# Performance work log

Hardware: AMD Instinct MI355X
Metric: run time of the kernel (lower is better)

The kernel has to match this reference:

```python
import jax, jax.numpy as jnp
import numpy as np

D_IN, D_K, D_V = 1024, 128, 128
B, S = 8, 4096


def setup_inputs() -> dict:
    key = jax.random.key(0)
    kq, kk, kv, kwq, kwk, kwv = jax.random.split(key, 6)
    q = jax.random.normal(kq, (B, S, D_IN), dtype=jnp.float32)
    k = jax.random.normal(kk, (B, S, D_IN), dtype=jnp.float32)
    v = jax.random.normal(kv, (B, S, D_IN), dtype=jnp.float32)
    # nn.Linear(d_in, d_out, bias=None): weight shape [d_out, d_in], y = x @ W^T
    scale = 1.0 / np.sqrt(D_IN)
    Wq = jax.random.uniform(kwq, (D_K, D_IN), jnp.float32, -scale, scale)
    Wk = jax.random.uniform(kwk, (D_K, D_IN), jnp.float32, -scale, scale)
    Wv = jax.random.uniform(kwv, (D_V, D_IN), jnp.float32, -scale, scale)
    return {"q": q, "k": k, "v": v, "Wq": Wq, "Wk": Wk, "Wv": Wv}


def reference(q, k, v, Wq, Wk, Wv):
    # Bias-free projections: [b, s, d_in] @ [d_in, d_k/d_v]
    qh = jnp.einsum('bsd,kd->bsk', q, Wq)
    kh = jnp.einsum('bsd,kd->bsk', k, Wk)
    vh = jnp.einsum('bsd,vd->bsv', v, Wv)
    scores = jnp.einsum('bqk,bsk->bqs', qh, kh) / jnp.sqrt(jnp.float32(D_K))
    attn = jax.nn.softmax(scores, axis=-1)  # [b, s_q, s_kv]
    return jnp.einsum('bqs,bsv->bqv', attn, vh)
```

## Files before the change

kernel.cpp:

```cpp
#include <hip/hip_runtime.h>
#include <hip/hip_bf16.h>
#include <stdint.h>

#define D_IN 1024
#define D_K  128
#define NBATCH 8
#define SEQ  4096
#define MROWS (NBATCH * SEQ)

typedef __attribute__((ext_vector_type(8))) short bf16x8;
typedef __attribute__((ext_vector_type(4))) float f32x4;

__device__ __forceinline__ unsigned short f32_to_bf16(float x) {
    union { float f; uint32_t u; } v; v.f = x;
    uint32_t r = 0x7FFFu + ((v.u >> 16) & 1u);
    return (unsigned short)((v.u + r) >> 16);
}

__device__ __forceinline__ bf16x8 cvt8(float4 lo, float4 hi) {
    bf16x8 r;
    r[0] = (short)f32_to_bf16(lo.x); r[1] = (short)f32_to_bf16(lo.y);
    r[2] = (short)f32_to_bf16(lo.z); r[3] = (short)f32_to_bf16(lo.w);
    r[4] = (short)f32_to_bf16(hi.x); r[5] = (short)f32_to_bf16(hi.y);
    r[6] = (short)f32_to_bf16(hi.z); r[7] = (short)f32_to_bf16(hi.w);
    return r;
}

__device__ __forceinline__ void gload16(const void* src, void* lds) {
    __builtin_amdgcn_global_load_lds(
        (const __attribute__((address_space(1))) void*)src,
        (__attribute__((address_space(3))) void*)lds, 16, 0, 0);
}

__global__ __launch_bounds__(256)
void wconv_kernel(const float* __restrict__ Wq, const float* __restrict__ Wk,
                  const float* __restrict__ Wv, unsigned short* __restrict__ Wt)
{
    const int t  = blockIdx.x * 256 + threadIdx.x;
    const int n  = t & 127;
    const int kc = (t >> 7) & 127;
    const int p  = t >> 14;
    const float* __restrict__ W = (p == 0) ? Wq : (p == 1) ? Wk : Wv;
    const float sc = (p == 0) ? (1.44269504088896f * 0.0883883476483184f) : 1.0f;
    const float4* src = reinterpret_cast<const float4*>(W + (size_t)n * D_IN + kc * 8);
    float4 a = src[0], b = src[1];
    uint4 o;
    o.x = (uint32_t)f32_to_bf16(a.x * sc) | ((uint32_t)f32_to_bf16(a.y * sc) << 16);
    o.y = (uint32_t)f32_to_bf16(a.z * sc) | ((uint32_t)f32_to_bf16(a.w * sc) << 16);
    o.z = (uint32_t)f32_to_bf16(b.x * sc) | ((uint32_t)f32_to_bf16(b.y * sc) << 16);
    o.w = (uint32_t)f32_to_bf16(b.z * sc) | ((uint32_t)f32_to_bf16(b.w * sc) << 16);
    *reinterpret_cast<uint4*>(Wt + (size_t)t * 8) = o;
}

#define RBM 32

__global__ __launch_bounds__(256, 3)
void proj_kernel(const float* __restrict__ Xq, const float* __restrict__ Xk,
                 const float* __restrict__ Xv,
                 const unsigned short* __restrict__ Wt,
                 unsigned short* __restrict__ qh, unsigned short* __restrict__ kh,
                 unsigned short* __restrict__ vhT)
{
    const int p = blockIdx.y;
    const float* __restrict__ X = (p == 0) ? Xq : (p == 1) ? Xk : Xv;
    const unsigned short* __restrict__ Wtp = Wt + (size_t)p * 128 * 128 * 8;

    __shared__ float Asf[RBM * 256];

    const int tid  = threadIdx.x;
    const int lane = tid & 63;
    const int w    = tid >> 6;
    const int lrow = lane & 15;
    const int g    = lane >> 4;
    const int wbase = blockIdx.x * RBM;

    f32x4 acc[2][2];
    #pragma unroll
    for (int mi = 0; mi < 2; ++mi)
        #pragma unroll
        for (int ni = 0; ni < 2; ++ni)
            acc[mi][ni] = (f32x4){0.f, 0.f, 0.f, 0.f};

    char* const abase0 = reinterpret_cast<char*>(Asf) + lrow * 1024;
    char* const abase1 = reinterpret_cast<char*>(Asf) + (16 + lrow) * 1024;
    const int aswz = (lrow & 7) << 5;
    bf16x8 bb[8];

    #pragma unroll
    for (int kk = 0; kk < 4; ++kk) {
        if (kk) __syncthreads();

        const unsigned short* __restrict__ wbk =
            Wtp + ((size_t)(kk * 32 + g) * 128 + w * 32 + lrow) * 8;
        #pragma unroll
        for (int s = 0; s < 4; ++s)
            #pragma unroll
            for (int ni = 0; ni < 2; ++ni)
                bb[s * 2 + ni] = *reinterpret_cast<const bf16x8*>(
                    wbk + ((size_t)(s * 4) * 128 + ni * 16) * 8);

        {
            const int r0 = w * 8;
            const char* src = reinterpret_cast<const char*>(
                X + (size_t)(wbase + r0) * D_IN + kk * 256) + lane * 16;
            float4 L0 = *reinterpret_cast<const float4*>(src);
            float4 L1 = *reinterpret_cast<const float4*>(src + 1 * 4096);
            float4 L2 = *reinterpret_cast<const float4*>(src + 2 * 4096);
            float4 L3 = *reinterpret_cast<const float4*>(src + 3 * 4096);
            float4 L4 = *reinterpret_cast<const float4*>(src + 4 * 4096);
            float4 L5 = *reinterpret_cast<const float4*>(src + 5 * 4096);
            float4 L6 = *reinterpret_cast<const float4*>(src + 6 * 4096);
            float4 L7 = *reinterpret_cast<const float4*>(src + 7 * 4096);
            char* const dst = reinterpret_cast<char*>(Asf);
            const int lb = lane * 16;
            #define WR(i, Li)                                                  \
            do {                                                               \
                const int r_ = r0 + (i);                                       \
                *reinterpret_cast<float4*>(dst + r_ * 1024 +                   \
                    (lb ^ ((r_ & 7) << 5))) = Li;                              \
            } while (0)
            WR(0, L0); WR(1, L1); WR(2, L2); WR(3, L3);
            WR(4, L4); WR(5, L5); WR(6, L6); WR(7, L7);
            #undef WR
        }
        __syncthreads();

        #pragma unroll
        for (int bt = 0; bt < 2; ++bt) {
            #pragma unroll
            for (int s = 0; s < 4; ++s) {
                const int t = bt * 4 + s;
                const int boff = (t * 128 + g * 32) ^ aswz;
                float4 lo0 = *reinterpret_cast<const float4*>(abase0 + boff);
                float4 hi0 = *reinterpret_cast<const float4*>(abase0 + boff + 16);
                float4 lo1 = *reinterpret_cast<const float4*>(abase1 + boff);
                float4 hi1 = *reinterpret_cast<const float4*>(abase1 + boff + 16);
                bf16x8 af0 = cvt8(lo0, hi0);
                bf16x8 af1 = cvt8(lo1, hi1);
                acc[0][0] = __builtin_amdgcn_mfma_f32_16x16x32_bf16(af0, bb[s * 2 + 0], acc[0][0], 0, 0, 0);
                acc[0][1] = __builtin_amdgcn_mfma_f32_16x16x32_bf16(af0, bb[s * 2 + 1], acc[0][1], 0, 0, 0);
                acc[1][0] = __builtin_amdgcn_mfma_f32_16x16x32_bf16(af1, bb[s * 2 + 0], acc[1][0], 0, 0, 0);
                acc[1][1] = __builtin_amdgcn_mfma_f32_16x16x32_bf16(af1, bb[s * 2 + 1], acc[1][1], 0, 0, 0);
                if (bt == 0) {
                    #pragma unroll
                    for (int ni = 0; ni < 2; ++ni)
                        bb[s * 2 + ni] = *reinterpret_cast<const bf16x8*>(
                            wbk + ((size_t)(16 + s * 4) * 128 + ni * 16) * 8);
                }
            }
        }
    }

    if (p < 2) {
        unsigned short* __restrict__ Y = (p == 0) ? qh : kh;
        #pragma unroll
        for (int mi = 0; mi < 2; ++mi) {
            const int rbase = wbase + mi * 16 + g * 4;
            #pragma unroll
            for (int ni = 0; ni < 2; ++ni) {
                const int n = w * 32 + ni * 16 + lrow;
                #pragma unroll
                for (int r = 0; r < 4; ++r)
                    Y[(size_t)(rbase + r) * D_K + n] = f32_to_bf16(acc[mi][ni][r]);
            }
        }
    } else {
        const int b = wbase >> 12;
        #pragma unroll
        for (int mi = 0; mi < 2; ++mi) {
            const int s = (wbase & 4095) + mi * 16 + g * 4;
            #pragma unroll
            for (int ni = 0; ni < 2; ++ni) {
                const int d = w * 32 + ni * 16 + lrow;
                uint2 t;
                t.x = (uint32_t)f32_to_bf16(acc[mi][ni][0]) |
                      ((uint32_t)f32_to_bf16(acc[mi][ni][1]) << 16);
                t.y = (uint32_t)f32_to_bf16(acc[mi][ni][2]) |
                      ((uint32_t)f32_to_bf16(acc[mi][ni][3]) << 16);
                *reinterpret_cast<uint2*>(vhT + ((size_t)(b * D_K + d) << 12) + s) = t;
            }
        }
    }
}

#define KVB 64

__global__ __launch_bounds__(256, 2)
void attn_kernel(const unsigned short* __restrict__ qh,
                 const unsigned short* __restrict__ kh,
                 const unsigned short* __restrict__ vhT,
                 float* __restrict__ out)
{
    __shared__ unsigned short Ks[2][KVB * D_K];
    __shared__ unsigned short Vs[2][D_K * KVB];
    __shared__ unsigned short Ps[4][16 * KVB];

    const int tid  = threadIdx.x;
    const int lane = tid & 63;
    const int wave = tid >> 6;
    const int b    = blockIdx.x & 7;
    const int qt   = blockIdx.x >> 3;
    const int q0   = qt * 64 + wave * 16;
    const int lrow = lane & 15;
    const int g4   = (lane >> 4) << 2;
    const int lk16 = (lane >> 4) * 16;

    const unsigned short* __restrict__ Kb = kh + (size_t)b * SEQ * D_K;
    const unsigned short* __restrict__ Vb = vhT + (size_t)b * D_K * SEQ;
    unsigned short* const Pw = Ps[wave];

    const int kr0  = lane >> 4;
    const int kcbp = (lane & 15) * 16;
    const int vr0  = lane >> 3;
    const int vcbp = (lane & 7) * 16;

    #define STAGE(buf, it_)                                                   \
    do {                                                                      \
        const int s0_ = (it_) * KVB;                                          \
        _Pragma("unroll")                                                     \
        for (int j = 0; j < 4; ++j) {                                         \
            const int blk  = wave * 4 + j;                                    \
            const int krow = blk * 4 + kr0;                                   \
            gload16(reinterpret_cast<const char*>(Kb) +                       \
                        (size_t)(s0_ + krow) * 256 +                          \
                        (kcbp ^ ((krow & 7) << 4)),                           \
                    reinterpret_cast<char*>(Ks[buf]) + blk * 1024);           \
            const int vrow = blk * 8 + vr0;                                   \
            gload16(reinterpret_cast<const char*>(Vb) +                       \
                        (size_t)vrow * (SEQ * 2) + (size_t)s0_ * 2 +          \
                        (vcbp ^ ((vrow & 7) << 4)),                           \
                    reinterpret_cast<char*>(Vs[buf]) + blk * 1024);           \
        }                                                                     \
    } while (0)

    bf16x8 qf[4];
    {
        const char* base = reinterpret_cast<const char*>(
            qh + (size_t)(b * SEQ + q0 + lrow) * D_K);
        #pragma unroll
        for (int ks = 0; ks < 4; ++ks)
            qf[ks] = *reinterpret_cast<const bf16x8*>(base + ks * 64 + lk16);
    }

    f32x4 o[8];
    #pragma unroll
    for (int df = 0; df < 8; ++df) o[df] = (f32x4){0.f, 0.f, 0.f, 0.f};
    float lsum[4] = {0.f, 0.f, 0.f, 0.f};

    STAGE(0, 0);
    asm volatile("s_waitcnt vmcnt(0)" ::: "memory");
    __syncthreads();

    int cur = 0;
    for (int it = 0; it < SEQ / KVB; ++it) {
        if (it + 1 < SEQ / KVB) STAGE(cur ^ 1, it + 1);

        f32x4 sc[4];
        #pragma unroll
        for (int sf = 0; sf < 4; ++sf) sc[sf] = (f32x4){0.f, 0.f, 0.f, 0.f};
        #pragma unroll
        for (int ks = 0; ks < 4; ++ks) {
            #pragma unroll
            for (int sf = 0; sf < 4; ++sf) {
                const int row = sf * 16 + lrow;
                bf16x8 kf = *reinterpret_cast<const bf16x8*>(
                    reinterpret_cast<const char*>(Ks[cur]) + row * 256 +
                    ((ks * 64 + lk16) ^ ((row & 7) << 4)));
                sc[sf] = __builtin_amdgcn_mfma_f32_16x16x32_bf16(qf[ks], kf, sc[sf], 0, 0, 0);
            }
        }

        #pragma unroll
        for (int sf = 0; sf < 4; ++sf) {
            #pragma unroll
            for (int r = 0; r < 4; ++r) {
                float pv = exp2f(sc[sf][r]);
                lsum[r] += pv;
                const int prow = g4 + r;
                const int pcol = (sf * 16 + lrow) * 2;
                *reinterpret_cast<unsigned short*>(
                    reinterpret_cast<char*>(Pw) + prow * 128 +
                    (pcol ^ ((prow & 7) << 4))) = f32_to_bf16(pv);
            }
        }

        #pragma unroll
        for (int ks = 0; ks < 2; ++ks) {
            bf16x8 pf = *reinterpret_cast<const bf16x8*>(
                reinterpret_cast<const char*>(Pw) + lrow * 128 +
                ((ks * 64 + lk16) ^ ((lrow & 7) << 4)));
            #pragma unroll
            for (int df = 0; df < 8; ++df) {
                const int vr = df * 16 + lrow;
                bf16x8 vf = *reinterpret_cast<const bf16x8*>(
                    reinterpret_cast<const char*>(Vs[cur]) + vr * 128 +
                    ((ks * 64 + lk16) ^ ((vr & 7) << 4)));
                o[df] = __builtin_amdgcn_mfma_f32_16x16x32_bf16(pf, vf, o[df], 0, 0, 0);
            }
        }

        asm volatile("s_waitcnt vmcnt(0)" ::: "memory");
        __syncthreads();
        cur ^= 1;
    }
    #undef STAGE

    #pragma unroll
    for (int r = 0; r < 4; ++r) {
        float s = lsum[r];
        s += __shfl_xor(s, 1);
        s += __shfl_xor(s, 2);
        s += __shfl_xor(s, 4);
        s += __shfl_xor(s, 8);
        float inv = 1.0f / s;
        const int row = q0 + g4 + r;
        float* ob = out + (size_t)(b * SEQ + row) * D_K + lrow;
        #pragma unroll
        for (int df = 0; df < 8; ++df)
            ob[df * 16] = o[df][r] * inv;
    }
}

extern "C" void kernel_launch(void* const* d_in, const int* in_sizes, int n_in,
                              void* d_out, int out_size, void* d_ws, size_t ws_size,
                              hipStream_t stream)
{
    (void)in_sizes; (void)n_in; (void)out_size; (void)ws_size;
    const float* q  = (const float*)d_in[0];
    const float* k  = (const float*)d_in[1];
    const float* v  = (const float*)d_in[2];
    const float* Wq = (const float*)d_in[3];
    const float* Wk = (const float*)d_in[4];
    const float* Wv = (const float*)d_in[5];

    unsigned short* qh  = (unsigned short*)d_ws;
    unsigned short* kh  = qh + (size_t)MROWS * D_K;
    unsigned short* vhT = kh + (size_t)MROWS * D_K;
    unsigned short* Wt  = vhT + (size_t)MROWS * D_K;

    wconv_kernel<<<dim3(192), 256, 0, stream>>>(Wq, Wk, Wv, Wt);
    proj_kernel<<<dim3(MROWS / RBM, 3), 256, 0, stream>>>(q, k, v, Wt, qh, kh, vhT);
    attn_kernel<<<dim3(NBATCH * (SEQ / 64)), 256, 0, stream>>>(qh, kh, vhT, (float*)d_out);
}
```

Before: 211.4 us.

## Transpose score MFMA so each lane writes packed P rows to padded LDS

Swaps the MFMA operands for the QK^T product so each lane holds four consecutive key scores for a single query row. Those four values are packed to bf16 with v_cvt_pk_bf16_f32 and written as one 8-byte store into a padded (144-byte stride) P buffer, replacing sixteen scalar 2-byte swizzled stores. Each lane now keeps one running row sum instead of four, and the final reduction uses cross-group shuffles plus a broadcast. This cuts LDS store count and conversion work per tile, at the cost of slightly more LDS for the padding.

```diff
diff --git a/kernel.cpp b/kernel.cpp
--- a/kernel.cpp
+++ b/kernel.cpp
@@ -184,6 +184,7 @@
 }
 
 #define KVB 64
+#define PSTRIDE 144
 
 __global__ __launch_bounds__(256, 2)
 void attn_kernel(const unsigned short* __restrict__ qh,
@@ -193,7 +194,7 @@
 {
     __shared__ unsigned short Ks[2][KVB * D_K];
     __shared__ unsigned short Vs[2][D_K * KVB];
-    __shared__ unsigned short Ps[4][16 * KVB];
+    __shared__ char Ps[4][16 * PSTRIDE];
 
     const int tid  = threadIdx.x;
     const int lane = tid & 63;
@@ -202,12 +203,13 @@
     const int qt   = blockIdx.x >> 3;
     const int q0   = qt * 64 + wave * 16;
     const int lrow = lane & 15;
-    const int g4   = (lane >> 4) << 2;
-    const int lk16 = (lane >> 4) * 16;
+    const int g    = lane >> 4;
+    const int g4   = g << 2;
+    const int lk16 = g * 16;
 
     const unsigned short* __restrict__ Kb = kh + (size_t)b * SEQ * D_K;
     const unsigned short* __restrict__ Vb = vhT + (size_t)b * D_K * SEQ;
-    unsigned short* const Pw = Ps[wave];
+    char* const Pw = Ps[wave];
 
     const int kr0  = lane >> 4;
     const int kcbp = (lane & 15) * 16;
@@ -245,7 +247,7 @@
     f32x4 o[8];
     #pragma unroll
     for (int df = 0; df < 8; ++df) o[df] = (f32x4){0.f, 0.f, 0.f, 0.f};
-    float lsum[4] = {0.f, 0.f, 0.f, 0.f};
+    float lsum = 0.f;
 
     STAGE(0, 0);
     asm volatile("s_waitcnt vmcnt(0)" ::: "memory");
@@ -255,9 +257,9 @@
     for (int it = 0; it < SEQ / KVB; ++it) {
         if (it + 1 < SEQ / KVB) STAGE(cur ^ 1, it + 1);
 
-        f32x4 sc[4];
-        #pragma unroll
-        for (int sf = 0; sf < 4; ++sf) sc[sf] = (f32x4){0.f, 0.f, 0.f, 0.f};
+        f32x4 scT[4];
+        #pragma unroll
+        for (int sf = 0; sf < 4; ++sf) scT[sf] = (f32x4){0.f, 0.f, 0.f, 0.f};
         #pragma unroll
         for (int ks = 0; ks < 4; ++ks) {
             #pragma unroll
@@ -266,29 +268,28 @@
                 bf16x8 kf = *reinterpret_cast<const bf16x8*>(
                     reinterpret_cast<const char*>(Ks[cur]) + row * 256 +
                     ((ks * 64 + lk16) ^ ((row & 7) << 4)));
-                sc[sf] = __builtin_amdgcn_mfma_f32_16x16x32_bf16(qf[ks], kf, sc[sf], 0, 0, 0);
+                scT[sf] = __builtin_amdgcn_mfma_f32_16x16x32_bf16(kf, qf[ks], scT[sf], 0, 0, 0);
             }
         }
 
         #pragma unroll
         for (int sf = 0; sf < 4; ++sf) {
-            #pragma unroll
-            for (int r = 0; r < 4; ++r) {
-                float pv = exp2f(sc[sf][r]);
-                lsum[r] += pv;
-                const int prow = g4 + r;
-                const int pcol = (sf * 16 + lrow) * 2;
-                *reinterpret_cast<unsigned short*>(
-                    reinterpret_cast<char*>(Pw) + prow * 128 +
-                    (pcol ^ ((prow & 7) << 4))) = f32_to_bf16(pv);
-            }
+            float p0 = exp2f(scT[sf][0]);
+            float p1 = exp2f(scT[sf][1]);
+            float p2 = exp2f(scT[sf][2]);
+            float p3 = exp2f(scT[sf][3]);
+            lsum += (p0 + p1) + (p2 + p3);
+            uint32_t u0, u1;
+            asm("v_cvt_pk_bf16_f32 %0, %1, %2" : "=v"(u0) : "v"(p0), "v"(p1));
+            asm("v_cvt_pk_bf16_f32 %0, %1, %2" : "=v"(u1) : "v"(p2), "v"(p3));
+            uint2 t; t.x = u0; t.y = u1;
+            *reinterpret_cast<uint2*>(Pw + lrow * PSTRIDE + (4 * sf + g) * 8) = t;
         }
 
         #pragma unroll
         for (int ks = 0; ks < 2; ++ks) {
             bf16x8 pf = *reinterpret_cast<const bf16x8*>(
-                reinterpret_cast<const char*>(Pw) + lrow * 128 +
-                ((ks * 64 + lk16) ^ ((lrow & 7) << 4)));
+                Pw + lrow * PSTRIDE + ks * 64 + g * 16);
             #pragma unroll
             for (int df = 0; df < 8; ++df) {
                 const int vr = df * 16 + lrow;
@@ -305,14 +306,12 @@
     }
     #undef STAGE
 
+    float s = lsum;
+    s += __shfl_xor(s, 16);
+    s += __shfl_xor(s, 32);
     #pragma unroll
     for (int r = 0; r < 4; ++r) {
-        float s = lsum[r];
-        s += __shfl_xor(s, 1);
-        s += __shfl_xor(s, 2);
-        s += __shfl_xor(s, 4);
-        s += __shfl_xor(s, 8);
-        float inv = 1.0f / s;
+        float inv = 1.0f / __shfl(s, g4 + r);
         const int row = q0 + g4 + r;
         float* ob = out + (size_t)(b * SEQ + row) * D_K + lrow;
         #pragma unroll
```

Result: faster. 205.0 us (-3.1%).
